# Performance work log

Hardware: AMD Instinct MI355X
Metric: run time of the kernel (lower is better)

Reference implementation:

```python
import jax, jax.numpy as jnp
import numpy as np

NUM_CLASSES = 80
STRIDES = (8, 16, 32)
REG_WEIGHT = 5.0


def _decode(o, stride):
    # o: [B, 5+num_classes, H, W] -> [B, H*W, 5+num_classes] with grid decode
    B, C, H, W = o.shape
    o = o.reshape(B, C, H * W).transpose(0, 2, 1)  # [B, HW, C]
    yv, xv = jnp.meshgrid(jnp.arange(H), jnp.arange(W), indexing='ij')
    grid = jnp.stack([xv, yv], axis=-1).reshape(1, H * W, 2).astype(o.dtype)
    xy = (o[..., :2] + grid) * stride
    wh = jnp.exp(o[..., 2:4]) * stride
    return jnp.concatenate([xy, wh, o[..., 4:]], axis=-1)


def _iou_loss(pred, target):
    # pred, target: [N,4] in cxcywh; IOUloss(loss_type='iou'): 1 - iou**2
    tl = jnp.maximum(pred[:, :2] - pred[:, 2:] / 2, target[:, :2] - target[:, 2:] / 2)
    br = jnp.minimum(pred[:, :2] + pred[:, 2:] / 2, target[:, :2] + target[:, 2:] / 2)
    area_p = jnp.prod(pred[:, 2:], axis=1)
    area_g = jnp.prod(target[:, 2:], axis=1)
    en = jnp.prod((tl < br).astype(pred.dtype), axis=1)
    area_i = jnp.prod(br - tl, axis=1) * en
    area_u = area_p + area_g - area_i
    iou = area_i / (area_u + 1e-16)
    return 1.0 - iou ** 2


def _bce_logits(x, t):
    # numerically stable BCEWithLogitsLoss(reduction='none')
    return jnp.maximum(x, 0.0) - x * t + jnp.log1p(jnp.exp(-jnp.abs(x)))


def _total_loss(out0, out1, out2, reg_targets, cls_targets, fg):
    outs = jnp.concatenate(
        [_decode(o, s) for o, s in zip((out0, out1, out2), STRIDES)], axis=1)
    bbox_preds = outs[..., :4]      # [B, A, 4] decoded cxcywh
    obj_preds = outs[..., 4]        # [B, A] logits
    cls_preds = outs[..., 5:]       # [B, A, num_classes] logits
    B, A, _ = bbox_preds.shape
    num_fg = jnp.maximum(fg.sum(), 1.0)
    iou_l = _iou_loss(bbox_preds.reshape(-1, 4), reg_targets.reshape(-1, 4)).reshape(B, A)
    loss_iou = (iou_l * fg).sum() / num_fg
    loss_obj = _bce_logits(obj_preds, fg).sum() / num_fg
    loss_cls = (_bce_logits(cls_preds, cls_targets) * fg[..., None]).sum() / num_fg
    return REG_WEIGHT * loss_iou + loss_obj + loss_cls


def setup_inputs() -> dict:
    key = jax.random.key(0)
    ks = jax.random.split(key, 6)
    B = 32
    A = 80 * 80 + 40 * 40 + 20 * 20  # 8400 anchors for 640x640 input
    out0 = jax.random.normal(ks[0], (B, 85, 80, 80), dtype=jnp.float32)
    out1 = jax.random.normal(ks[1], (B, 85, 40, 40), dtype=jnp.float32)
    out2 = jax.random.normal(ks[2], (B, 85, 20, 20), dtype=jnp.float32)
    # cxcywh targets in image coords (640x640), wh strictly positive
    reg_targets = jax.random.uniform(ks[3], (B, A, 4), dtype=jnp.float32) * 300.0 + 1.0
    cls_targets = jax.random.uniform(ks[4], (B, A, 80), dtype=jnp.float32)
    fg_mask = jax.random.randint(ks[5], (B, A), 0, 2, dtype=jnp.int32)
    return {'out0': out0, 'out1': out1, 'out2': out2,
            'reg_targets': reg_targets, 'cls_targets': cls_targets,
            'fg_mask': fg_mask}


def reference(out0, out1, out2, reg_targets, cls_targets, fg_mask):
    fg = fg_mask.astype(out0.dtype)
    return _total_loss(out0, out1, out2, reg_targets, cls_targets, fg)
```

## Files before the change

### kernel.cpp

```cpp
#include <hip/hip_runtime.h>
#include <math.h>

constexpr int A_TOTAL = 8400;

__device__ __forceinline__ float bce(float x, float t) {
    return fmaxf(x, 0.0f) - x * t + log1pf(expf(-fabsf(x)));
}

__global__ __launch_bounds__(256) void yolox_main(
    const float* __restrict__ out0, const float* __restrict__ out1,
    const float* __restrict__ out2, const float* __restrict__ regt,
    const float* __restrict__ clst, const int* __restrict__ fgm,
    double* __restrict__ acc, int B)
{
    int g = blockIdx.x * blockDim.x + threadIdx.x;
    float local = 0.0f, fgl = 0.0f;
    int total = B * A_TOTAL;
    if (g < total) {
        int b = g / A_TOTAL;
        int r = g - b * A_TOTAL;
        const float* obase; int HW; float stride; int a, gx, gy;
        if (r < 6400) {
            obase = out0 + (size_t)b * 85 * 6400; HW = 6400; stride = 8.0f;
            a = r;        gx = a % 80; gy = a / 80;
        } else if (r < 8000) {
            obase = out1 + (size_t)b * 85 * 1600; HW = 1600; stride = 16.0f;
            a = r - 6400; gx = a % 40; gy = a / 40;
        } else {
            obase = out2 + (size_t)b * 85 * 400;  HW = 400;  stride = 32.0f;
            a = r - 8000; gx = a % 20; gy = a / 20;
        }
        float tx   = obase[a];
        float ty   = obase[(size_t)1 * HW + a];
        float tw   = obase[(size_t)2 * HW + a];
        float th   = obase[(size_t)3 * HW + a];
        float tobj = obase[(size_t)4 * HW + a];

        float px = (tx + (float)gx) * stride;
        float py = (ty + (float)gy) * stride;
        float pw = expf(tw) * stride;
        float ph = expf(th) * stride;

        float4 t = reinterpret_cast<const float4*>(regt)[g];
        float fgv = (float)fgm[g];

        float tlx = fmaxf(px - pw * 0.5f, t.x - t.z * 0.5f);
        float tly = fmaxf(py - ph * 0.5f, t.y - t.w * 0.5f);
        float brx = fminf(px + pw * 0.5f, t.x + t.z * 0.5f);
        float bry = fminf(py + ph * 0.5f, t.y + t.w * 0.5f);
        float area_p = pw * ph;
        float area_g = t.z * t.w;
        float en = ((tlx < brx) && (tly < bry)) ? 1.0f : 0.0f;
        float area_i = (brx - tlx) * (bry - tly) * en;
        float area_u = area_p + area_g - area_i;
        float iou = area_i / (area_u + 1e-16f);
        float l_iou = 1.0f - iou * iou;

        local = 5.0f * l_iou * fgv + bce(tobj, fgv);
        fgl = fgv;

        if (fgv != 0.0f) {
            const float* cp = obase + (size_t)5 * HW + a;
            const float4* ct = reinterpret_cast<const float4*>(clst) + (size_t)g * 20;
            float cl = 0.0f;
            #pragma unroll 5
            for (int c4 = 0; c4 < 20; ++c4) {
                float4 tv = ct[c4];
                float x0 = cp[(size_t)(4 * c4 + 0) * HW];
                float x1 = cp[(size_t)(4 * c4 + 1) * HW];
                float x2 = cp[(size_t)(4 * c4 + 2) * HW];
                float x3 = cp[(size_t)(4 * c4 + 3) * HW];
                cl += bce(x0, tv.x) + bce(x1, tv.y) + bce(x2, tv.z) + bce(x3, tv.w);
            }
            local += cl * fgv;
        }
    }

    for (int off = 32; off > 0; off >>= 1) {
        local += __shfl_down(local, off, 64);
        fgl   += __shfl_down(fgl,   off, 64);
    }
    __shared__ float s_loss[4], s_fg[4];
    int wid  = threadIdx.x >> 6;
    int lane = threadIdx.x & 63;
    if (lane == 0) { s_loss[wid] = local; s_fg[wid] = fgl; }
    __syncthreads();
    if (threadIdx.x == 0) {
        float bl = s_loss[0] + s_loss[1] + s_loss[2] + s_loss[3];
        float bf = s_fg[0]   + s_fg[1]   + s_fg[2]   + s_fg[3];
        atomicAdd(&acc[0], (double)bl);
        atomicAdd(&acc[1], (double)bf);
    }
}

__global__ void yolox_final(const double* __restrict__ acc, float* __restrict__ out) {
    out[0] = (float)(acc[0] / fmax(acc[1], 1.0));
}

extern "C" void kernel_launch(void* const* d_in, const int* in_sizes, int n_in,
                              void* d_out, int out_size, void* d_ws, size_t ws_size,
                              hipStream_t stream) {
    const float* out0 = (const float*)d_in[0];
    const float* out1 = (const float*)d_in[1];
    const float* out2 = (const float*)d_in[2];
    const float* regt = (const float*)d_in[3];
    const float* clst = (const float*)d_in[4];
    const int*   fgm  = (const int*)d_in[5];

    int B = in_sizes[0] / (85 * 6400);
    double* acc = (double*)d_ws;
    hipMemsetAsync(acc, 0, 2 * sizeof(double), stream);

    int total  = B * A_TOTAL;
    int blocks = (total + 255) / 256;
    hipLaunchKernelGGL(yolox_main, dim3(blocks), dim3(256), 0, stream,
                       out0, out1, out2, regt, clst, fgm, acc, B);
    hipLaunchKernelGGL(yolox_final, dim3(1), dim3(1), 0, stream, acc, (float*)d_out);
}
```

Measured before the change: 237.1 us.

## Split class BCE into separate kernel with four threads per anchor, use fast math

Moves the IoU and objectness terms into one kernel and the class BCE into a second kernel, where four threads each handle 20 of the 80 classes of one anchor. This raises parallelism and memory-level concurrency for the dominant class-loss traffic, and reduces divergence when only some anchors are foreground. The class kernel's per-thread reads of the target row are 80-byte chunks. BCE and decode also switch to __expf and __logf intrinsics, trading some accuracy for cheaper transcendentals. The cost is an extra launch, re-reading fg_mask, and a second round of block atomics.

```diff
diff --git a/kernel.cpp b/kernel.cpp
--- a/kernel.cpp
+++ b/kernel.cpp
@@ -4,14 +4,36 @@
 constexpr int A_TOTAL = 8400;
 
 __device__ __forceinline__ float bce(float x, float t) {
-    return fmaxf(x, 0.0f) - x * t + log1pf(expf(-fabsf(x)));
+    float ax = fabsf(x);
+    float sp = __logf(1.0f + __expf(-ax));
+    return fmaxf(x, 0.0f) - x * t + sp;
 }
 
-__global__ __launch_bounds__(256) void yolox_main(
+__device__ __forceinline__ void block_reduce_atomic(float v, float w, double* acc,
+                                                    bool two) {
+    for (int off = 32; off > 0; off >>= 1) {
+        v += __shfl_down(v, off, 64);
+        if (two) w += __shfl_down(w, off, 64);
+    }
+    __shared__ float s_v[4], s_w[4];
+    int wid  = threadIdx.x >> 6;
+    int lane = threadIdx.x & 63;
+    if (lane == 0) { s_v[wid] = v; s_w[wid] = w; }
+    __syncthreads();
+    if (threadIdx.x == 0) {
+        float bv = s_v[0] + s_v[1] + s_v[2] + s_v[3];
+        atomicAdd(&acc[0], (double)bv);
+        if (two) {
+            float bw = s_w[0] + s_w[1] + s_w[2] + s_w[3];
+            atomicAdd(&acc[1], (double)bw);
+        }
+    }
+}
+
+__global__ __launch_bounds__(256) void yolox_iou_obj(
     const float* __restrict__ out0, const float* __restrict__ out1,
     const float* __restrict__ out2, const float* __restrict__ regt,
-    const float* __restrict__ clst, const int* __restrict__ fgm,
-    double* __restrict__ acc, int B)
+    const int* __restrict__ fgm, double* __restrict__ acc, int B)
 {
     int g = blockIdx.x * blockDim.x + threadIdx.x;
     float local = 0.0f, fgl = 0.0f;
@@ -38,8 +60,8 @@
 
         float px = (tx + (float)gx) * stride;
         float py = (ty + (float)gy) * stride;
-        float pw = expf(tw) * stride;
-        float ph = expf(th) * stride;
+        float pw = __expf(tw) * stride;
+        float ph = __expf(th) * stride;
 
         float4 t = reinterpret_cast<const float4*>(regt)[g];
         float fgv = (float)fgm[g];
@@ -58,39 +80,48 @@
 
         local = 5.0f * l_iou * fgv + bce(tobj, fgv);
         fgl = fgv;
+    }
+    block_reduce_atomic(local, fgl, acc, true);
+}
 
-        if (fgv != 0.0f) {
-            const float* cp = obase + (size_t)5 * HW + a;
-            const float4* ct = reinterpret_cast<const float4*>(clst) + (size_t)g * 20;
+__global__ __launch_bounds__(256) void yolox_cls(
+    const float* __restrict__ out0, const float* __restrict__ out1,
+    const float* __restrict__ out2, const float* __restrict__ clst,
+    const int* __restrict__ fgm, double* __restrict__ acc, int B)
+{
+    int t = blockIdx.x * blockDim.x + threadIdx.x;
+    float local = 0.0f;
+    int total4 = B * A_TOTAL * 4;
+    if (t < total4) {
+        int g = t >> 2;
+        int q = t & 3;
+        if (fgm[g] != 0) {
+            int b = g / A_TOTAL;
+            int r = g - b * A_TOTAL;
+            const float* cp; int HW; int a;
+            if (r < 6400) {
+                cp = out0 + (size_t)b * 85 * 6400 + (size_t)5 * 6400; HW = 6400; a = r;
+            } else if (r < 8000) {
+                cp = out1 + (size_t)b * 85 * 1600 + (size_t)5 * 1600; HW = 1600; a = r - 6400;
+            } else {
+                cp = out2 + (size_t)b * 85 * 400  + (size_t)5 * 400;  HW = 400;  a = r - 8000;
+            }
+            cp += a + (size_t)(q * 20) * HW;
+            const float4* ct = reinterpret_cast<const float4*>(clst + (size_t)g * 80 + q * 20);
             float cl = 0.0f;
-            #pragma unroll 5
-            for (int c4 = 0; c4 < 20; ++c4) {
-                float4 tv = ct[c4];
-                float x0 = cp[(size_t)(4 * c4 + 0) * HW];
-                float x1 = cp[(size_t)(4 * c4 + 1) * HW];
-                float x2 = cp[(size_t)(4 * c4 + 2) * HW];
-                float x3 = cp[(size_t)(4 * c4 + 3) * HW];
+            #pragma unroll
+            for (int i = 0; i < 5; ++i) {
+                float4 tv = ct[i];
+                float x0 = cp[(size_t)(4 * i + 0) * HW];
+                float x1 = cp[(size_t)(4 * i + 1) * HW];
+                float x2 = cp[(size_t)(4 * i + 2) * HW];
+                float x3 = cp[(size_t)(4 * i + 3) * HW];
                 cl += bce(x0, tv.x) + bce(x1, tv.y) + bce(x2, tv.z) + bce(x3, tv.w);
             }
-            local += cl * fgv;
+            local = cl;
         }
     }
-
-    for (int off = 32; off > 0; off >>= 1) {
-        local += __shfl_down(local, off, 64);
-        fgl   += __shfl_down(fgl,   off, 64);
-    }
-    __shared__ float s_loss[4], s_fg[4];
-    int wid  = threadIdx.x >> 6;
-    int lane = threadIdx.x & 63;
-    if (lane == 0) { s_loss[wid] = local; s_fg[wid] = fgl; }
-    __syncthreads();
-    if (threadIdx.x == 0) {
-        float bl = s_loss[0] + s_loss[1] + s_loss[2] + s_loss[3];
-        float bf = s_fg[0]   + s_fg[1]   + s_fg[2]   + s_fg[3];
-        atomicAdd(&acc[0], (double)bl);
-        atomicAdd(&acc[1], (double)bf);
-    }
+    block_reduce_atomic(local, 0.0f, acc, false);
 }
 
 __global__ void yolox_final(const double* __restrict__ acc, float* __restrict__ out) {
@@ -112,8 +143,11 @@
     hipMemsetAsync(acc, 0, 2 * sizeof(double), stream);
 
     int total  = B * A_TOTAL;
-    int blocks = (total + 255) / 256;
-    hipLaunchKernelGGL(yolox_main, dim3(blocks), dim3(256), 0, stream,
-                       out0, out1, out2, regt, clst, fgm, acc, B);
+    int blocks1 = (total + 255) / 256;
+    int blocks2 = (total * 4 + 255) / 256;
+    hipLaunchKernelGGL(yolox_iou_obj, dim3(blocks1), dim3(256), 0, stream,
+                       out0, out1, out2, regt, fgm, acc, B);
+    hipLaunchKernelGGL(yolox_cls, dim3(blocks2), dim3(256), 0, stream,
+                       out0, out1, out2, clst, fgm, acc, B);
     hipLaunchKernelGGL(yolox_final, dim3(1), dim3(1), 0, stream, acc, (float*)d_out);
 }
```

New measurement: 235.2 us. About the same (-0.8%).

## Split class loss over four lanes per anchor quad with float4 loads, fast math

Applied to the files above, without the earlier changes.

Remaps the work so that each group of four threads handles four adjacent anchors. Each thread loads a 20-class slice of logits as float4 vectors along the spatial dimension, so the strided per-class scalar reads become coalesced vector loads. The branch that skipped class work for background anchors is removed, so all anchors now compute the class BCE and multiply by the mask. This trades the skipped work for uniform, fully vectorized memory access. The exp and log calls are also switched to fast intrinsics, which adds some precision risk.

```diff
diff --git a/kernel.cpp b/kernel.cpp
--- a/kernel.cpp
+++ b/kernel.cpp
@@ -2,94 +2,113 @@
 #include <math.h>
 
 constexpr int A_TOTAL = 8400;
+constexpr int AGPI    = A_TOTAL / 4;
 
 __device__ __forceinline__ float bce(float x, float t) {
-    return fmaxf(x, 0.0f) - x * t + log1pf(expf(-fabsf(x)));
+    float ax = fabsf(x);
+    float sp = __logf(1.0f + __expf(-ax));
+    return fmaxf(x, 0.0f) - x * t + sp;
 }
 
-__global__ __launch_bounds__(256) void yolox_main(
+__device__ __forceinline__ float get4(const float4& v, int j) {
+    return j == 0 ? v.x : (j == 1 ? v.y : (j == 2 ? v.z : v.w));
+}
+
+__global__ __launch_bounds__(256) void yolox_fused(
     const float* __restrict__ out0, const float* __restrict__ out1,
     const float* __restrict__ out2, const float* __restrict__ regt,
     const float* __restrict__ clst, const int* __restrict__ fgm,
     double* __restrict__ acc, int B)
 {
-    int g = blockIdx.x * blockDim.x + threadIdx.x;
-    float local = 0.0f, fgl = 0.0f;
-    int total = B * A_TOTAL;
-    if (g < total) {
-        int b = g / A_TOTAL;
-        int r = g - b * A_TOTAL;
-        const float* obase; int HW; float stride; int a, gx, gy;
-        if (r < 6400) {
-            obase = out0 + (size_t)b * 85 * 6400; HW = 6400; stride = 8.0f;
-            a = r;        gx = a % 80; gy = a / 80;
-        } else if (r < 8000) {
-            obase = out1 + (size_t)b * 85 * 1600; HW = 1600; stride = 16.0f;
-            a = r - 6400; gx = a % 40; gy = a / 40;
-        } else {
-            obase = out2 + (size_t)b * 85 * 400;  HW = 400;  stride = 32.0f;
-            a = r - 8000; gx = a % 20; gy = a / 20;
+    int t  = blockIdx.x * blockDim.x + threadIdx.x;
+    int q  = t & 3;
+    int ag = t >> 2;
+    int b  = ag / AGPI;
+    int rg = ag - b * AGPI;
+    int a0 = rg * 4;
+
+    const float* obase; int HW; float stride; int al; int W;
+    if (a0 < 6400)      { obase = out0 + (size_t)b * 85 * 6400; HW = 6400; stride = 8.0f;  al = a0;        W = 80; }
+    else if (a0 < 8000) { obase = out1 + (size_t)b * 85 * 1600; HW = 1600; stride = 16.0f; al = a0 - 6400; W = 40; }
+    else                { obase = out2 + (size_t)b * 85 * 400;  HW = 400;  stride = 32.0f; al = a0 - 8000; W = 20; }
+
+    float4 L[20];
+    const float* cb = obase + (size_t)(5 + q * 20) * HW + al;
+    #pragma unroll
+    for (int i = 0; i < 20; ++i)
+        L[i] = *reinterpret_cast<const float4*>(cb + (size_t)i * HW);
+
+    int4 fg4 = *reinterpret_cast<const int4*>(fgm + (size_t)b * A_TOTAL + a0);
+    float fgf[4] = { (float)fg4.x, (float)fg4.y, (float)fg4.z, (float)fg4.w };
+
+    float local = 0.0f;
+    #pragma unroll
+    for (int j = 0; j < 4; ++j) {
+        const float4* tp = reinterpret_cast<const float4*>(
+            clst + ((size_t)b * A_TOTAL + a0 + j) * 80 + q * 20);
+        float tg[20];
+        #pragma unroll
+        for (int i5 = 0; i5 < 5; ++i5) {
+            float4 tv = tp[i5];
+            tg[4 * i5 + 0] = tv.x; tg[4 * i5 + 1] = tv.y;
+            tg[4 * i5 + 2] = tv.z; tg[4 * i5 + 3] = tv.w;
         }
-        float tx   = obase[a];
-        float ty   = obase[(size_t)1 * HW + a];
-        float tw   = obase[(size_t)2 * HW + a];
-        float th   = obase[(size_t)3 * HW + a];
-        float tobj = obase[(size_t)4 * HW + a];
+        float s = 0.0f;
+        #pragma unroll
+        for (int i = 0; i < 20; ++i)
+            s += bce(get4(L[i], j), tg[i]);
+        local += s * fgf[j];
+    }
+
+    {
+        int aa  = al + q;
+        int a   = a0 + q;
+        int gx  = a % W == a % W ? (aa % W) : 0;
+        gx = aa % W;
+        int gy  = aa / W;
+        float tx   = obase[aa];
+        float ty   = obase[(size_t)1 * HW + aa];
+        float tw   = obase[(size_t)2 * HW + aa];
+        float th   = obase[(size_t)3 * HW + aa];
+        float tobj = obase[(size_t)4 * HW + aa];
 
         float px = (tx + (float)gx) * stride;
         float py = (ty + (float)gy) * stride;
-        float pw = expf(tw) * stride;
-        float ph = expf(th) * stride;
+        float pw = __expf(tw) * stride;
+        float ph = __expf(th) * stride;
 
-        float4 t = reinterpret_cast<const float4*>(regt)[g];
-        float fgv = (float)fgm[g];
+        float4 rt = reinterpret_cast<const float4*>(regt)[(size_t)b * A_TOTAL + a];
+        float fgv = get4(make_float4(fgf[0], fgf[1], fgf[2], fgf[3]), q);
 
-        float tlx = fmaxf(px - pw * 0.5f, t.x - t.z * 0.5f);
-        float tly = fmaxf(py - ph * 0.5f, t.y - t.w * 0.5f);
-        float brx = fminf(px + pw * 0.5f, t.x + t.z * 0.5f);
-        float bry = fminf(py + ph * 0.5f, t.y + t.w * 0.5f);
+        float tlx = fmaxf(px - pw * 0.5f, rt.x - rt.z * 0.5f);
+        float tly = fmaxf(py - ph * 0.5f, rt.y - rt.w * 0.5f);
+        float brx = fminf(px + pw * 0.5f, rt.x + rt.z * 0.5f);
+        float bry = fminf(py + ph * 0.5f, rt.y + rt.w * 0.5f);
         float area_p = pw * ph;
-        float area_g = t.z * t.w;
+        float area_g = rt.z * rt.w;
         float en = ((tlx < brx) && (tly < bry)) ? 1.0f : 0.0f;
         float area_i = (brx - tlx) * (bry - tly) * en;
         float area_u = area_p + area_g - area_i;
         float iou = area_i / (area_u + 1e-16f);
         float l_iou = 1.0f - iou * iou;
 
-        local = 5.0f * l_iou * fgv + bce(tobj, fgv);
-        fgl = fgv;
+        local += 5.0f * l_iou * fgv + bce(tobj, fgv);
 
-        if (fgv != 0.0f) {
-            const float* cp = obase + (size_t)5 * HW + a;
-            const float4* ct = reinterpret_cast<const float4*>(clst) + (size_t)g * 20;
-            float cl = 0.0f;
-            #pragma unroll 5
-            for (int c4 = 0; c4 < 20; ++c4) {
-                float4 tv = ct[c4];
-                float x0 = cp[(size_t)(4 * c4 + 0) * HW];
-                float x1 = cp[(size_t)(4 * c4 + 1) * HW];
-                float x2 = cp[(size_t)(4 * c4 + 2) * HW];
-                float x3 = cp[(size_t)(4 * c4 + 3) * HW];
-                cl += bce(x0, tv.x) + bce(x1, tv.y) + bce(x2, tv.z) + bce(x3, tv.w);
-            }
-            local += cl * fgv;
+        float fgl = fgv;
+
+        for (int off = 32; off > 0; off >>= 1) {
+            local += __shfl_down(local, off, 64);
+            fgl   += __shfl_down(fgl,   off, 64);
         }
-    }
-
-    for (int off = 32; off > 0; off >>= 1) {
-        local += __shfl_down(local, off, 64);
-        fgl   += __shfl_down(fgl,   off, 64);
-    }
-    __shared__ float s_loss[4], s_fg[4];
-    int wid  = threadIdx.x >> 6;
-    int lane = threadIdx.x & 63;
-    if (lane == 0) { s_loss[wid] = local; s_fg[wid] = fgl; }
-    __syncthreads();
-    if (threadIdx.x == 0) {
-        float bl = s_loss[0] + s_loss[1] + s_loss[2] + s_loss[3];
-        float bf = s_fg[0]   + s_fg[1]   + s_fg[2]   + s_fg[3];
-        atomicAdd(&acc[0], (double)bl);
-        atomicAdd(&acc[1], (double)bf);
+        __shared__ float s_v[4], s_w[4];
+        int wid  = threadIdx.x >> 6;
+        int lane = threadIdx.x & 63;
+        if (lane == 0) { s_v[wid] = local; s_w[wid] = fgl; }
+        __syncthreads();
+        if (threadIdx.x == 0) {
+            atomicAdd(&acc[0], (double)(s_v[0] + s_v[1] + s_v[2] + s_v[3]));
+            atomicAdd(&acc[1], (double)(s_w[0] + s_w[1] + s_w[2] + s_w[3]));
+        }
     }
 }
 
@@ -113,7 +132,7 @@
 
     int total  = B * A_TOTAL;
     int blocks = (total + 255) / 256;
-    hipLaunchKernelGGL(yolox_main, dim3(blocks), dim3(256), 0, stream,
+    hipLaunchKernelGGL(yolox_fused, dim3(blocks), dim3(256), 0, stream,
                        out0, out1, out2, regt, clst, fgm, acc, B);
     hipLaunchKernelGGL(yolox_final, dim3(1), dim3(1), 0, stream, acc, (float*)d_out);
 }
```

Measured after the change: 208.0 us. -12.3%, faster.
